# Kernel tuning notes

Measured on AMD Instinct MI355X. Metric: run time of the kernel, lower is better.

Reference implementation:

```python
import jax, jax.numpy as jnp
import numpy as np

VOCAB = 50257
F = 1024
RANK = 8


def setup_inputs() -> dict:
    key = jax.random.key(0)
    k_idx, k_emb, k_a = jax.random.split(key, 3)
    index_tensor = jax.random.randint(k_idx, (8, 4096), 0, VOCAB, dtype=jnp.int64)
    emb_weight = jax.random.normal(k_emb, (VOCAB, F), dtype=jnp.float32)
    # kaiming_uniform_ with nonlinearity='linear': bound = sqrt(3)*sqrt(1/fan_in), fan_in=RANK
    bound = float(np.sqrt(3.0) * np.sqrt(1.0 / RANK))
    A = jax.random.uniform(k_a, (F, RANK), minval=-bound, maxval=bound, dtype=jnp.float32)
    B = jnp.zeros((RANK, F), dtype=jnp.float32)
    bias = jnp.zeros((F,), dtype=jnp.float32)
    return {"index_tensor": index_tensor, "emb_weight": emb_weight, "A": A, "B": B, "bias": bias}


def reference(index_tensor, emb_weight, A, B, bias):
    # base = E[idx]; out = base @ (I + A@B) + bias == base + (base@A)@B + bias
    base = emb_weight[index_tensor]                      # [b, s, F] gather
    low = jnp.einsum('bsf,fr->bsr', base, A)             # [b, s, R]
    return base + jnp.einsum('bsr,rf->bsf', low, B) + bias
```

## Files before the change

### kernel.cpp

```cpp
#include <hip/hip_runtime.h>


constexpr int F = 1024;
constexpr int R = 8;
constexpr int TOKS_PER_BLOCK = 16;
constexpr int TPB = TOKS_PER_BLOCK * 64;

__global__ __launch_bounds__(TPB)
void lora_embedding_kernel(const int* __restrict__ idx,
                           const float* __restrict__ emb,
                           const float* __restrict__ A,
                           const float* __restrict__ Bm,
                           const float* __restrict__ bias,
                           float* __restrict__ out,
                           int ntok)
{
    __shared__ float sAT[R][F];
    __shared__ float sB[R][F];

    const int t = threadIdx.x;

    {
        const float4* A4 = reinterpret_cast<const float4*>(A);
        const float4* B4 = reinterpret_cast<const float4*>(Bm);
        float4* sB4 = reinterpret_cast<float4*>(&sB[0][0]);
        #pragma unroll
        for (int i = 0; i < (F * R / 4) / TPB; ++i) {
            const int n4 = t + i * TPB;
            const float4 a = A4[n4];
            const int f0 = n4 >> 1;
            const int r0 = (n4 & 1) * 4;
            sAT[r0 + 0][f0] = a.x;
            sAT[r0 + 1][f0] = a.y;
            sAT[r0 + 2][f0] = a.z;
            sAT[r0 + 3][f0] = a.w;
            sB4[n4] = B4[n4];
        }
    }
    __syncthreads();

    const int wave = t >> 6;
    const int lane = t & 63;
    const int tok = blockIdx.x * TOKS_PER_BLOCK + wave;
    if (tok >= ntok) return;

    const int row = idx[tok];
    const float4* src = reinterpret_cast<const float4*>(emb + (size_t)row * F);

    float4 v[4];
    #pragma unroll
    for (int k = 0; k < 4; ++k) v[k] = src[lane + 64 * k];

    float p[R];
    #pragma unroll
    for (int r = 0; r < R; ++r) {
        float s = 0.f;
        #pragma unroll
        for (int k = 0; k < 4; ++k) {
            const float4 a =
                *reinterpret_cast<const float4*>(&sAT[r][4 * (lane + 64 * k)]);
            s += v[k].x * a.x + v[k].y * a.y + v[k].z * a.z + v[k].w * a.w;
        }
        #pragma unroll
        for (int off = 32; off >= 1; off >>= 1)
            s += __shfl_xor(s, off, 64);
        p[r] = s;
    }

    float4* dst = reinterpret_cast<float4*>(out + (size_t)tok * F);
    const float4* bias4 = reinterpret_cast<const float4*>(bias);
    #pragma unroll
    for (int k = 0; k < 4; ++k) {
        const int q = lane + 64 * k;
        float4 o = v[k];
        const float4 bi = bias4[q];
        o.x += bi.x; o.y += bi.y; o.z += bi.z; o.w += bi.w;
        #pragma unroll
        for (int r = 0; r < R; ++r) {
            const float4 b =
                *reinterpret_cast<const float4*>(&sB[r][4 * q]);
            o.x += p[r] * b.x;
            o.y += p[r] * b.y;
            o.z += p[r] * b.z;
            o.w += p[r] * b.w;
        }
        dst[q] = o;
    }
}

extern "C" void kernel_launch(void* const* d_in, const int* in_sizes, int n_in,
                              void* d_out, int out_size, void* d_ws, size_t ws_size,
                              hipStream_t stream) {
    const int*   idx  = (const int*)  d_in[0];
    const float* emb  = (const float*)d_in[1];
    const float* A    = (const float*)d_in[2];
    const float* Bm   = (const float*)d_in[3];
    const float* bias = (const float*)d_in[4];
    float* out = (float*)d_out;

    const int ntok = in_sizes[0];
    const int blocks = (ntok + TOKS_PER_BLOCK - 1) / TOKS_PER_BLOCK;

    hipLaunchKernelGGL(lora_embedding_kernel, dim3(blocks), dim3(TPB), 0, stream,
                       idx, emb, A, Bm, bias, out, ntok);
}
```

Before: 316.5 us.

## Use persistent blocks with register-resident LoRA weights and prefetched token rows

```diff
diff --git a/kernel.cpp b/kernel.cpp
--- a/kernel.cpp
+++ b/kernel.cpp
@@ -1,90 +1,127 @@
 #include <hip/hip_runtime.h>
 
 
-constexpr int F = 1024;
-constexpr int R = 8;
-constexpr int TOKS_PER_BLOCK = 16;
-constexpr int TPB = TOKS_PER_BLOCK * 64;
+constexpr int F  = 1024;
+constexpr int R  = 8;
+constexpr int F4 = F / 4;
+constexpr int TPB  = 256;
+constexpr int NBLK = 2048;
 
-__global__ __launch_bounds__(TPB)
-void lora_embedding_kernel(const int* __restrict__ idx,
-                           const float* __restrict__ emb,
-                           const float* __restrict__ A,
-                           const float* __restrict__ Bm,
-                           const float* __restrict__ bias,
-                           float* __restrict__ out,
-                           int ntok)
+__global__ __launch_bounds__(TPB, 4)
+void lora_emb_kernel(const int* __restrict__ idx,
+                     const float* __restrict__ emb,
+                     const float* __restrict__ A,
+                     const float* __restrict__ Bm,
+                     const float* __restrict__ bias,
+                     float* __restrict__ out,
+                     int ntok)
 {
-    __shared__ float sAT[R][F];
-    __shared__ float sB[R][F];
+    __shared__ float ldsP[2][4][R];
 
-    const int t = threadIdx.x;
+    const int lane    = threadIdx.x & 63;
+    const int quarter = threadIdx.x >> 6;
+    const int f4      = quarter * 64 + lane;
 
-    {
-        const float4* A4 = reinterpret_cast<const float4*>(A);
-        const float4* B4 = reinterpret_cast<const float4*>(Bm);
-        float4* sB4 = reinterpret_cast<float4*>(&sB[0][0]);
+    float a_frag[4][8];
+    #pragma unroll
+    for (int j = 0; j < 4; ++j) {
+        const float* ap = A + (size_t)(4 * f4 + j) * R;
+        const float4 lo = *reinterpret_cast<const float4*>(ap);
+        const float4 hi = *reinterpret_cast<const float4*>(ap + 4);
+        a_frag[j][0] = lo.x; a_frag[j][1] = lo.y; a_frag[j][2] = lo.z; a_frag[j][3] = lo.w;
+        a_frag[j][4] = hi.x; a_frag[j][5] = hi.y; a_frag[j][6] = hi.z; a_frag[j][7] = hi.w;
+    }
+    float b_frag[8][4];
+    #pragma unroll
+    for (int r = 0; r < 8; ++r) {
+        const float4 b = *reinterpret_cast<const float4*>(Bm + (size_t)r * F + 4 * f4);
+        b_frag[r][0] = b.x; b_frag[r][1] = b.y; b_frag[r][2] = b.z; b_frag[r][3] = b.w;
+    }
+    const float4 bi = *reinterpret_cast<const float4*>(bias + 4 * f4);
+
+    const float4* emb4 = reinterpret_cast<const float4*>(emb);
+    float4*       out4 = reinterpret_cast<float4*>(out);
+
+    const int stride = gridDim.x;
+    int t = blockIdx.x;
+    if (t >= ntok) return;
+
+    int   t1      = t + stride;
+    int   row_nxt = (t1 < ntok) ? idx[t1] : 0;
+    float4 v      = emb4[(size_t)idx[t] * F4 + f4];
+
+    const bool s1 = (lane & 1) != 0;
+    const bool s2 = (lane & 2) != 0;
+    const bool s4 = (lane & 4) != 0;
+    const int  rr = ((lane & 1) << 2) | (lane & 2) | ((lane >> 2) & 1);
+
+    int buf = 0;
+    while (true) {
+        const bool hasn = (t1 < ntok);
+        float4 vn;
+        if (hasn) vn = emb4[(size_t)row_nxt * F4 + f4];
+        const int t2     = t1 + stride;
+        const int row_n2 = (t2 < ntok) ? idx[t2] : 0;
+
+        float p[8];
         #pragma unroll
-        for (int i = 0; i < (F * R / 4) / TPB; ++i) {
-            const int n4 = t + i * TPB;
-            const float4 a = A4[n4];
-            const int f0 = n4 >> 1;
-            const int r0 = (n4 & 1) * 4;
-            sAT[r0 + 0][f0] = a.x;
-            sAT[r0 + 1][f0] = a.y;
-            sAT[r0 + 2][f0] = a.z;
-            sAT[r0 + 3][f0] = a.w;
-            sB4[n4] = B4[n4];
+        for (int r = 0; r < 8; ++r)
+            p[r] = v.x * a_frag[0][r] + v.y * a_frag[1][r]
+                 + v.z * a_frag[2][r] + v.w * a_frag[3][r];
+
+        float q[4];
+        #pragma unroll
+        for (int j = 0; j < 4; ++j) {
+            const float send = s1 ? p[j]     : p[j + 4];
+            const float keep = s1 ? p[j + 4] : p[j];
+            q[j] = keep + __shfl_xor(send, 1, 64);
         }
-    }
-    __syncthreads();
+        float w2[2];
+        #pragma unroll
+        for (int j = 0; j < 2; ++j) {
+            const float send = s2 ? q[j]     : q[j + 2];
+            const float keep = s2 ? q[j + 2] : q[j];
+            w2[j] = keep + __shfl_xor(send, 2, 64);
+        }
+        float s = (s4 ? w2[1] : w2[0]) + __shfl_xor(s4 ? w2[0] : w2[1], 4, 64);
+        s += __shfl_xor(s, 8, 64);
+        s += __shfl_xor(s, 16, 64);
+        s += __shfl_xor(s, 32, 64);
 
-    const int wave = t >> 6;
-    const int lane = t & 63;
-    const int tok = blockIdx.x * TOKS_PER_BLOCK + wave;
-    if (tok >= ntok) return;
+        if (lane < 8) ldsP[buf][quarter][rr] = s;
+        __syncthreads();
 
-    const int row = idx[tok];
-    const float4* src = reinterpret_cast<const float4*>(emb + (size_t)row * F);
+        float pall[8];
+        {
+            const float4* pb = reinterpret_cast<const float4*>(&ldsP[buf][0][0]);
+            const float4 l0 = pb[0], h0 = pb[1];
+            const float4 l1 = pb[2], h1 = pb[3];
+            const float4 l2 = pb[4], h2 = pb[5];
+            const float4 l3 = pb[6], h3 = pb[7];
+            pall[0] = l0.x + l1.x + l2.x + l3.x;
+            pall[1] = l0.y + l1.y + l2.y + l3.y;
+            pall[2] = l0.z + l1.z + l2.z + l3.z;
+            pall[3] = l0.w + l1.w + l2.w + l3.w;
+            pall[4] = h0.x + h1.x + h2.x + h3.x;
+            pall[5] = h0.y + h1.y + h2.y + h3.y;
+            pall[6] = h0.z + h1.z + h2.z + h3.z;
+            pall[7] = h0.w + h1.w + h2.w + h3.w;
+        }
 
-    float4 v[4];
-    #pragma unroll
-    for (int k = 0; k < 4; ++k) v[k] = src[lane + 64 * k];
+        const float vv[4] = { v.x, v.y, v.z, v.w };
+        const float bb[4] = { bi.x, bi.y, bi.z, bi.w };
+        float o[4];
+        #pragma unroll
+        for (int c = 0; c < 4; ++c) {
+            float acc = vv[c] + bb[c];
+            #pragma unroll
+            for (int r = 0; r < 8; ++r) acc += pall[r] * b_frag[r][c];
+            o[c] = acc;
+        }
+        out4[(size_t)t * F4 + f4] = make_float4(o[0], o[1], o[2], o[3]);
 
-    float p[R];
-    #pragma unroll
-    for (int r = 0; r < R; ++r) {
-        float s = 0.f;
-        #pragma unroll
-        for (int k = 0; k < 4; ++k) {
-            const float4 a =
-                *reinterpret_cast<const float4*>(&sAT[r][4 * (lane + 64 * k)]);
-            s += v[k].x * a.x + v[k].y * a.y + v[k].z * a.z + v[k].w * a.w;
-        }
-        #pragma unroll
-        for (int off = 32; off >= 1; off >>= 1)
-            s += __shfl_xor(s, off, 64);
-        p[r] = s;
-    }
-
-    float4* dst = reinterpret_cast<float4*>(out + (size_t)tok * F);
-    const float4* bias4 = reinterpret_cast<const float4*>(bias);
-    #pragma unroll
-    for (int k = 0; k < 4; ++k) {
-        const int q = lane + 64 * k;
-        float4 o = v[k];
-        const float4 bi = bias4[q];
-        o.x += bi.x; o.y += bi.y; o.z += bi.z; o.w += bi.w;
-        #pragma unroll
-        for (int r = 0; r < R; ++r) {
-            const float4 b =
-                *reinterpret_cast<const float4*>(&sB[r][4 * q]);
-            o.x += p[r] * b.x;
-            o.y += p[r] * b.y;
-            o.z += p[r] * b.z;
-            o.w += p[r] * b.w;
-        }
-        dst[q] = o;
+        if (!hasn) break;
+        v = vn; t = t1; t1 = t2; row_nxt = row_n2; buf ^= 1;
     }
 }
 
@@ -99,8 +136,9 @@
     float* out = (float*)d_out;
 
     const int ntok = in_sizes[0];
-    const int blocks = (ntok + TOKS_PER_BLOCK - 1) / TOKS_PER_BLOCK;
+    int blocks = NBLK;
+    if (blocks > ntok) blocks = ntok;
 
-    hipLaunchKernelGGL(lora_embedding_kernel, dim3(blocks), dim3(TPB), 0, stream,
+    hipLaunchKernelGGL(lora_emb_kernel, dim3(blocks), dim3(TPB), 0, stream,
                        idx, emb, A, Bm, bias, out, ntok);
 }
```

New measurement: 323.0 us. 1.02x slower.
